# Kernel optimization log

Hardware: AMD Instinct MI355X
Metric: run time of the kernel (lower is better)

## Reference

```python
import jax, jax.numpy as jnp
import numpy as np

H = 128            # hardcoded image side in the torch module
TOL = 1e-3         # forward() default tol
MAX_DEPTH = 8      # init kwarg (reduced from 200 for bounded runtime)
LRELU = 0.1        # LeakyReLU negative slope


def _conv(x, w, b, pad):
    # x: [B,Cin,H,H], w: [Cout,Cin,kh,kw]
    y = jax.lax.conv_general_dilated(
        x, w, (1, 1), [(pad, pad), (pad, pad)],
        dimension_numbers=('NCHW', 'OIHW', 'NCHW'))
    if b is not None:
        y = y + b[None, :, None, None]
    return y


def _leaky(x):
    return jnp.where(x >= 0, x, LRELU * x)


def _build_apply_T(d, A, w1, b1, w2, b2, w3, b3, wK, delta, alpha, lambd, beta):
    B = d.shape[0]
    Kc = wK.shape[0]
    dcol = d.reshape(B, -1).T                      # [m, B]
    # ConvTranspose2d(K->1, k=3, pad=1) with weight := convK.weight is the
    # adjoint of convK: regular conv with spatially flipped, channel-swapped kernel.
    wKt = jnp.transpose(jnp.flip(wK, (2, 3)), (1, 0, 2, 3))  # [1,K,3,3]

    def K_op(xk):                                  # [N,B] -> [K*N,B]
        x4 = xk.T.reshape(B, 1, H, H)
        return _conv(x4, wK, None, 1).reshape(B, -1).T

    def Kt_op(pk):                                 # [K*N,B] -> [N,B]
        p4 = pk.T.reshape(B, Kc, H, H)
        return _conv(p4, wKt, None, 1).reshape(B, -1).T

    def R_op(pk):                                  # learned residual denoiser
        p = pk.T.reshape(B, Kc, H, H)
        p = p + _leaky(_conv(p, w1, b1, 2))
        p = p + _leaky(_conv(p, w2, b2, 2))
        p = p + _leaky(_conv(p, w3, b3, 2))
        return p.reshape(B, -1).T

    def ball_proj(w):                              # eval-mode projection
        de = jnp.exp(delta)                        # (1,) -> broadcasts over batch
        dist = jnp.maximum(jnp.linalg.norm(w - dcol, axis=0), 1e-10)
        dn = jnp.linalg.norm(dcol, axis=0)
        scale = jnp.minimum(jnp.ones_like(dist), de * dn / dist)
        return dcol + scale * (w - dcol)

    a = jnp.clip(alpha, 0.0, 2.0)
    bta = jnp.clip(beta, 0.0, 2.0)
    lam = jnp.clip(lambd, 0.0, 2.0)

    def apply_T(x):                                # x: [B,1,H,H]
        xk = x.reshape(B, -1).T                    # [N,B]
        Kxk = K_op(xk)
        # torch: pk = K(xk); pk += lambd*(nuk1 + alpha*(K(xk)-pk)) with nuk1=0
        # and pk==K(xk), so the update is identity -> pk = Kxk.
        pk = R_op(Kxk)
        Axk = A @ xk                               # [m,B]
        # torch: wk = A@xk; temp = wk + lambd*(nuk2 + alpha*(Axk-wk)) = Axk.
        wk = ball_proj(Axk)
        nuk1p = a * (Kxk - pk)
        nuk2p = a * (Axk - wk)
        # nuk1 = nuk2 = 0, so 2*nuk_plus - nuk = 2*nuk_plus
        rk = Kt_op(2.0 * nuk1p) + A.T @ (2.0 * nuk2p)
        xk_new = jnp.clip(xk - bta * rk, 0.0, 1.0)
        return xk_new.T.reshape(B, 1, H, H)

    return apply_T


def setup_inputs() -> dict:
    key = jax.random.key(0)
    ks = jax.random.split(key, 10)
    B, M, N_side, Kc = 8, 4096, 128, 2
    d = jax.random.normal(ks[0], (B, M), jnp.float32)
    A = jax.random.normal(ks[1], (M, N_side * N_side), jnp.float32) / 128.0
    w1 = jax.random.normal(ks[2], (Kc, Kc, 5, 5), jnp.float32) * 0.05
    w2 = jax.random.normal(ks[3], (Kc, Kc, 5, 5), jnp.float32) * 0.05
    w3 = jax.random.normal(ks[4], (Kc, Kc, 5, 5), jnp.float32) * 0.05
    b1 = jnp.zeros((Kc,), jnp.float32)
    b2 = jnp.zeros((Kc,), jnp.float32)
    b3 = jnp.zeros((Kc,), jnp.float32)
    wK = jax.random.normal(ks[5], (Kc, 1, 3, 3), jnp.float32) * 0.1
    return {
        'd': d, 'A': A,
        'w1': w1, 'b1': b1, 'w2': w2, 'b2': b2, 'w3': w3, 'b3': b3,
        'wK': wK,
        'delta': jnp.full((1,), -5.0, jnp.float32),
        'alpha': jnp.full((1,), 0.1, jnp.float32),
        'lambd': jnp.full((1,), 0.1, jnp.float32),
        'beta': jnp.full((1,), 0.1, jnp.float32),
    }


def reference(d, A, w1, b1, w2, b2, w3, b3, wK, delta, alpha, lambd, beta):
    B = d.shape[0]
    apply_T = _build_apply_T(d, A, w1, b1, w2, b2, w3, b3, wK,
                             delta, alpha, lambd, beta)
    x0 = jnp.zeros((B, 1, H, H), d.dtype)
    xp0 = jnp.full((B, 1, H, H), jnp.inf, d.dtype)

    def cond(state):
        x, xp, k = state
        res = jnp.max(jnp.linalg.norm((x - xp).reshape(B, -1), axis=1))
        return (res > TOL) & (k < MAX_DEPTH)

    def body(state):
        x, xp, k = state
        return (apply_T(x), x, k + 1)

    x_star, _, _ = jax.lax.while_loop(cond, body, (x0, xp0, jnp.int32(0)))
    # final differentiable application T(x*)
    return apply_T(x_star)
```

## Files before the change

kernel.cpp:

```cpp
#include <hip/hip_runtime.h>
#include <math.h>

#define HH 128
#define NPIX 16384
#define BB 8
#define MM 4096
#define NN 16384
#define LRELU_S 0.1f

typedef __attribute__((ext_vector_type(8))) short bf16x8;
typedef __attribute__((ext_vector_type(4))) float f32x4;

__device__ __forceinline__ float leaky_(float v){ return v >= 0.f ? v : LRELU_S*v; }
__device__ __forceinline__ float clamp01(float v){ return fminf(fmaxf(v, 0.f), 1.f); }
__device__ __forceinline__ float clamp02(float v){ return fminf(fmaxf(v, 0.f), 2.f); }
__device__ __forceinline__ unsigned short f2bf(float f){
  unsigned u = __float_as_uint(f);
  u = (u + 0x7FFFu + ((u >> 16) & 1u)) >> 16;
  return (unsigned short)u;
}
__device__ __forceinline__ float bf2f(unsigned short s){
  return __uint_as_float(((unsigned)s) << 16);
}

__global__ __launch_bounds__(256) void k_prep_pack(const float* __restrict__ A_,
                                                   unsigned short* __restrict__ Apk){
  __shared__ unsigned short lb[16][1032];
  int blk = blockIdx.x;
  int mt = blk >> 4, ch = blk & 15;
  int t = threadIdx.x;
  #pragma unroll
  for (int i=0;i<16;++i){
    float4 v = *(const float4*)&A_[(size_t)(mt*16+i)*NN + ch*1024 + t*4];
    unsigned short o[4] = {f2bf(v.x),f2bf(v.y),f2bf(v.z),f2bf(v.w)};
    *(uint2*)&lb[i][t*4] = *(uint2*)o;
  }
  __syncthreads();
  size_t base = ((size_t)mt*2048 + ch*128)*128;
  #pragma unroll
  for (int j=0;j<8;++j){
    int o = j*256 + t;
    int k8l = o >> 4, col = o & 15;
    uint4 v = *(const uint4*)&lb[col][k8l*8];
    *(uint4*)&Apk[base + (size_t)o*8] = v;
  }
}

__global__ __launch_bounds__(256) void k_dn(const float* __restrict__ d, float* __restrict__ dn){
  int b = blockIdx.x, t = threadIdx.x;
  float ss = 0.f;
  for (int m=t; m<MM; m+=256){ float v = d[b*MM + m]; ss += v*v; }
  #pragma unroll
  for (int off=32; off; off>>=1) ss += __shfl_down(ss, off);
  __shared__ float red[4];
  if ((t & 63) == 0) red[t>>6] = ss;
  __syncthreads();
  if (t == 0) dn[b] = sqrtf(red[0]+red[1]+red[2]+red[3]);
}

__global__ __launch_bounds__(256) void k_gemm1p(const unsigned short* __restrict__ Apk,
    const unsigned short* __restrict__ xtt, float* __restrict__ e_part){
  __shared__ float part[4][16][16];
  int blk = blockIdx.x;
  int mt = blk >> 2, ng = blk & 3;
  int t = threadIdx.x, w = t >> 6, lane = t & 63;
  int kg = lane >> 4, col = lane & 15;
  const unsigned short* Ap = Apk + (((size_t)mt*2048 + ng*512 + w*128 + kg)*16 + col)*8;
  const unsigned short* Bp = xtt + ((size_t)(ng*512 + w*128 + kg)*16 + col)*8;
  f32x4 acc = {0.f,0.f,0.f,0.f};
  #pragma unroll 8
  for (int s=0; s<32; ++s){
    bf16x8 a = *(const bf16x8*)(Ap + s*512);
    bf16x8 b = *(const bf16x8*)(Bp + s*512);
    acc = __builtin_amdgcn_mfma_f32_16x16x32_bf16(a, b, acc, 0, 0, 0);
  }
  #pragma unroll
  for (int j=0;j<4;++j) part[w][kg*4+j][col] = acc[j];
  __syncthreads();
  int r = t >> 4, b = t & 15;
  float s = part[0][r][b] + part[1][r][b] + part[2][r][b] + part[3][r][b];
  e_part[((size_t)ng*MM + mt*16 + r)*16 + b] = s;
}

__global__ __launch_bounds__(256) void k_conv_chain(const float* __restrict__ x,
    const float* __restrict__ wK, const float* __restrict__ w1, const float* __restrict__ b1,
    const float* __restrict__ w2, const float* __restrict__ b2,
    const float* __restrict__ w3, const float* __restrict__ b3,
    const float* __restrict__ alpha, float* __restrict__ rk){
  __shared__ float xs[24][128];
  __shared__ float bufA[2][22][128];
  __shared__ float bufB[2][18][128];
  __shared__ float wKs[18], w1s[100], w2s[100], w3s[100], bs[3][2];
  __shared__ float twoa;
  int blk = blockIdx.x;
  int b = blk >> 4, slab = blk & 15, r0 = slab*8;
  int t = threadIdx.x;
  for (int i=t;i<18;i+=256) wKs[i]=wK[i];
  for (int i=t;i<100;i+=256){ w1s[i]=w1[i]; w2s[i]=w2[i]; w3s[i]=w3[i]; }
  if (t<2){ bs[0][t]=b1[t]; bs[1][t]=b2[t]; bs[2][t]=b3[t]; }
  if (t==0) twoa = 2.f*clamp02(alpha[0]);
  for (int idx=t; idx<24*128; idx+=256){
    int i = idx>>7, j = idx&127, ir = r0-8+i;
    xs[i][j] = ((unsigned)ir < 128u) ? x[b*NPIX + ir*HH + j] : 0.f;
  }
  __syncthreads();
  for (int c=0;c<2;++c)
    for (int idx=t; idx<22*128; idx+=256){
      int i = idx>>7, j = idx&127, ir = r0-7+i;
      float s = 0.f;
      if ((unsigned)ir < 128u){
        #pragma unroll
        for (int di=0;di<3;++di)
          #pragma unroll
          for (int dj=0;dj<3;++dj){
            int jj = j+dj-1;
            if ((unsigned)jj < 128u) s += xs[i+di][jj]*wKs[(c*3+di)*3+dj];
          }
      }
      bufA[c][i][j] = s;
    }
  __syncthreads();
  for (int o=0;o<2;++o)
    for (int idx=t; idx<18*128; idx+=256){
      int i = idx>>7, j = idx&127, ir = r0-5+i;
      float v = 0.f;
      if ((unsigned)ir < 128u){
        float s = bs[0][o];
        #pragma unroll
        for (int c=0;c<2;++c)
          #pragma unroll
          for (int di=0;di<5;++di)
            #pragma unroll
            for (int dj=0;dj<5;++dj){
              int jj = j+dj-2;
              if ((unsigned)jj < 128u) s += bufA[c][i+di][jj]*w1s[(o*2+c)*25+di*5+dj];
            }
        v = bufA[o][i+2][j] + leaky_(s);
      }
      bufB[o][i][j] = v;
    }
  __syncthreads();
  for (int o=0;o<2;++o)
    for (int idx=t; idx<14*128; idx+=256){
      int i = idx>>7, j = idx&127, ir = r0-3+i;
      float v = 0.f;
      if ((unsigned)ir < 128u){
        float s = bs[1][o];
        #pragma unroll
        for (int c=0;c<2;++c)
          #pragma unroll
          for (int di=0;di<5;++di)
            #pragma unroll
            for (int dj=0;dj<5;++dj){
              int jj = j+dj-2;
              if ((unsigned)jj < 128u) s += bufB[c][i+di][jj]*w2s[(o*2+c)*25+di*5+dj];
            }
        v = bufB[o][i+2][j] + leaky_(s);
      }
      bufA[o][i][j] = v;
    }
  __syncthreads();
  for (int o=0;o<2;++o)
    for (int idx=t; idx<10*128; idx+=256){
      int i = idx>>7, j = idx&127, ir = r0-1+i;
      float v = 0.f;
      if ((unsigned)ir < 128u){
        float s = bs[2][o];
        #pragma unroll
        for (int c=0;c<2;++c)
          #pragma unroll
          for (int di=0;di<5;++di)
            #pragma unroll
            for (int dj=0;dj<5;++dj){
              int jj = j+dj-2;
              if ((unsigned)jj < 128u) s += bufA[c][i+di][jj]*w3s[(o*2+c)*25+di*5+dj];
            }
        v = bufA[o][i+2][j] + leaky_(s);
      }
      bufB[o][i][j] = v;
    }
  __syncthreads();
  for (int c=0;c<2;++c)
    for (int idx=t; idx<10*128; idx+=256){
      int i = idx>>7, j = idx&127, ir = r0-1+i;
      float v = 0.f;
      if ((unsigned)ir < 128u){
        float kx = 0.f;
        #pragma unroll
        for (int di=0;di<3;++di)
          #pragma unroll
          for (int dj=0;dj<3;++dj){
            int jj = j+dj-1;
            if ((unsigned)jj < 128u) kx += xs[i+6+di][jj]*wKs[(c*3+di)*3+dj];
          }
        v = twoa*(kx - bufB[c][i][j]);
      }
      bufA[c][i][j] = v;
    }
  __syncthreads();
  for (int idx=t; idx<8*128; idx+=256){
    int i = idx>>7, j = idx&127, ir = r0+i;
    float s = 0.f;
    #pragma unroll
    for (int c=0;c<2;++c)
      #pragma unroll
      for (int di=0;di<3;++di)
        #pragma unroll
        for (int dj=0;dj<3;++dj){
          int jj = j+dj-1;
          if ((unsigned)jj < 128u) s += bufA[c][i+di][jj]*wKs[(c*3+(2-di))*3+(2-dj)];
        }
    rk[b*NPIX + ir*HH + j] = s;
  }
}

__global__ __launch_bounds__(256) void k_gemm2a(const unsigned short* __restrict__ Apk,
    const float* __restrict__ e_part, const float* __restrict__ d_,
    float* __restrict__ up, float* __restrict__ d2p){
  __shared__ float zs[8][512];
  __shared__ float red8s[64];
  int blk = blockIdx.x;
  int msp = blk >> 8, nb = blk & 255;
  int m0 = msp*512, mt0 = msp*32, k80 = nb*8;
  int t = threadIdx.x;
  for (int i=t; i<4096; i+=256){
    int ml = i >> 3, b = i & 7;
    int m = m0 + ml;
    float s = e_part[(size_t)(0*MM + m)*16 + b]
            + e_part[(size_t)(1*MM + m)*16 + b]
            + e_part[(size_t)(2*MM + m)*16 + b]
            + e_part[(size_t)(3*MM + m)*16 + b];
    zs[b][ml] = s - d_[b*MM + m];
  }
  __syncthreads();
  if (nb == 0){
    if (t < 64){
      int b = t & 7, g = t >> 3;
      float s = 0.f;
      #pragma unroll
      for (int i=0;i<64;++i){ float v = zs[b][g*64+i]; s += v*v; }
      red8s[g*8 + b] = s;
    }
    __syncthreads();
    if (t < 8){
      float s2 = 0.f;
      #pragma unroll
      for (int g=0;g<8;++g) s2 += red8s[g*8 + t];
      d2p[msp*8 + t] = s2;
    }
  }
  int col = t & 15, ehalf = (t >> 4) & 1, k8l = t >> 5;
  int k8 = k80 + k8l;
  const unsigned short* Ap = Apk + ((((size_t)mt0*2048 + k8)*16 + col)*8 + ehalf*4);
  float acc[8][4];
  #pragma unroll
  for (int b=0;b<8;++b)
    #pragma unroll
    for (int e=0;e<4;++e) acc[b][e] = 0.f;
  for (int mb=0; mb<32; mb+=4){
    uint2 a4[4];
    #pragma unroll
    for (int u=0;u<4;++u)
      a4[u] = *(const uint2*)(Ap + (size_t)(mb+u)*262144);
    #pragma unroll
    for (int u=0;u<4;++u){
      float av[4];
      av[0] = bf2f((unsigned short)(a4[u].x & 0xffff));
      av[1] = bf2f((unsigned short)(a4[u].x >> 16));
      av[2] = bf2f((unsigned short)(a4[u].y & 0xffff));
      av[3] = bf2f((unsigned short)(a4[u].y >> 16));
      int ml = (mb+u)*16 + col;
      #pragma unroll
      for (int b=0;b<8;++b){
        float z = zs[b][ml];
        acc[b][0] += av[0]*z; acc[b][1] += av[1]*z;
        acc[b][2] += av[2]*z; acc[b][3] += av[3]*z;
      }
    }
  }
  #pragma unroll
  for (int mask=1; mask<16; mask<<=1)
    #pragma unroll
    for (int b=0;b<8;++b)
      #pragma unroll
      for (int e=0;e<4;++e) acc[b][e] += __shfl_xor(acc[b][e], mask);
  if (col < 8){
    int b = col;
    float4 v = {acc[b][0], acc[b][1], acc[b][2], acc[b][3]};
    *(float4*)&up[((size_t)msp*8 + b)*NN + k8*8 + ehalf*4] = v;
  }
}

__global__ __launch_bounds__(256) void k_combine3(const float* __restrict__ up,
    const float* __restrict__ rk1, const float* __restrict__ d2p,
    const float* __restrict__ dn, const float* __restrict__ delta,
    const float* __restrict__ alpha, const float* __restrict__ beta,
    float* __restrict__ x, unsigned short* __restrict__ xtt){
  __shared__ float cf_s[8];
  int t = threadIdx.x;
  if (t < 8){
    float s2 = 0.f;
    #pragma unroll
    for (int ms=0; ms<8; ++ms) s2 += d2p[ms*8 + t];
    float dist = fmaxf(sqrtf(s2), 1e-10f);
    float de = expf(delta[0]);
    float a = clamp02(alpha[0]);
    cf_s[t] = 2.f*a*(1.f - fminf(1.f, de*dn[t]/dist));
  }
  __syncthreads();
  float bta = clamp02(beta[0]);
  int o = blockIdx.x*256 + t;
  int b = o >> 14, pix = o & 16383;
  float s = 0.f;
  #pragma unroll
  for (int p=0; p<8; ++p)
    s += up[((size_t)p*8 + b)*NN + pix];
  float tot = rk1[b*NPIX + pix] + cf_s[b]*s;
  float xn = clamp01(x[b*NPIX + pix] - bta*tot);
  x[b*NPIX + pix] = xn;
  xtt[((size_t)(pix>>3)*16 + b)*8 + (pix&7)] = f2bf(xn);
}

extern "C" void kernel_launch(void* const* d_in, const int* in_sizes, int n_in,
                              void* d_out, int out_size, void* d_ws, size_t ws_size,
                              hipStream_t stream) {
  const float* d_d   = (const float*)d_in[0];
  const float* d_A   = (const float*)d_in[1];
  const float* w1    = (const float*)d_in[2];
  const float* b1    = (const float*)d_in[3];
  const float* w2    = (const float*)d_in[4];
  const float* b2    = (const float*)d_in[5];
  const float* w3    = (const float*)d_in[6];
  const float* b3    = (const float*)d_in[7];
  const float* wK    = (const float*)d_in[8];
  const float* delta = (const float*)d_in[9];
  const float* alpha = (const float*)d_in[10];
  const float* beta  = (const float*)d_in[12];

  char* p = (char*)d_ws;
  unsigned short* Apk = (unsigned short*)p; p += (size_t)MM*NN*2;
  unsigned short* xtt = (unsigned short*)p; p += (size_t)2048*16*8*2;
  float* x      = (float*)p; p += (size_t)BB*NPIX*4;
  float* rk1    = (float*)p; p += (size_t)BB*NPIX*4;
  float* e_part = (float*)p; p += (size_t)4*MM*16*4;
  float* up     = (float*)p; p += (size_t)8*8*NN*4;
  float* d2p    = (float*)p; p += (size_t)8*8*4;
  float* dnb    = (float*)p; p += 64;

  k_prep_pack<<<4096, 256, 0, stream>>>(d_A, Apk);
  k_dn<<<BB, 256, 0, stream>>>(d_d, dnb);
  hipMemsetAsync(x, 0, (size_t)BB*NPIX*4, stream);
  hipMemsetAsync(xtt, 0, (size_t)2048*16*8*2, stream);

  for (int it=0; it<9; ++it){
    k_conv_chain<<<128, 256, 0, stream>>>(x, wK, w1, b1, w2, b2, w3, b3, alpha, rk1);
    k_gemm1p<<<1024, 256, 0, stream>>>(Apk, xtt, e_part);
    k_gemm2a<<<2048, 256, 0, stream>>>(Apk, e_part, d_d, up, d2p);
    k_combine3<<<512, 256, 0, stream>>>(up, rk1, d2p, dnb, delta, alpha, beta, x, xtt);
  }

  hipMemcpyAsync(d_out, x, (size_t)BB*NPIX*4, hipMemcpyDeviceToDevice, stream);
}
```

Before: 1.492 ms.

## Merge conv chain with GEMM1 in one launch, store conv buffers as bf16, widen GEMM2 tiles

The denoiser conv chain and the first GEMM now run as one launch, with block ranges split between the two roles, so one launch is removed per iteration and both can run concurrently. The conv chain's shared-memory intermediates are stored as bf16 to shrink LDS use, which allows higher occupancy but lowers precision in the residual chain. GEMM2 now gives each thread 8 output columns instead of 4, which halves the grid and makes the A loads wider, at the cost of more accumulator registers.

```diff
diff --git a/kernel.cpp b/kernel.cpp
--- a/kernel.cpp
+++ b/kernel.cpp
@@ -58,50 +58,56 @@
   if (t == 0) dn[b] = sqrtf(red[0]+red[1]+red[2]+red[3]);
 }
 
-__global__ __launch_bounds__(256) void k_gemm1p(const unsigned short* __restrict__ Apk,
-    const unsigned short* __restrict__ xtt, float* __restrict__ e_part){
-  __shared__ float part[4][16][16];
-  int blk = blockIdx.x;
-  int mt = blk >> 2, ng = blk & 3;
-  int t = threadIdx.x, w = t >> 6, lane = t & 63;
-  int kg = lane >> 4, col = lane & 15;
-  const unsigned short* Ap = Apk + (((size_t)mt*2048 + ng*512 + w*128 + kg)*16 + col)*8;
-  const unsigned short* Bp = xtt + ((size_t)(ng*512 + w*128 + kg)*16 + col)*8;
-  f32x4 acc = {0.f,0.f,0.f,0.f};
-  #pragma unroll 8
-  for (int s=0; s<32; ++s){
-    bf16x8 a = *(const bf16x8*)(Ap + s*512);
-    bf16x8 b = *(const bf16x8*)(Bp + s*512);
-    acc = __builtin_amdgcn_mfma_f32_16x16x32_bf16(a, b, acc, 0, 0, 0);
-  }
-  #pragma unroll
-  for (int j=0;j<4;++j) part[w][kg*4+j][col] = acc[j];
-  __syncthreads();
-  int r = t >> 4, b = t & 15;
-  float s = part[0][r][b] + part[1][r][b] + part[2][r][b] + part[3][r][b];
-  e_part[((size_t)ng*MM + mt*16 + r)*16 + b] = s;
-}
-
-__global__ __launch_bounds__(256) void k_conv_chain(const float* __restrict__ x,
+#define XS(i,j)   xsB[(i)*128+(j)]
+#define BA(c,i,j) bufAB[((c)*22+(i))*128+(j)]
+#define BBD(c,i,j) bufBB[((c)*18+(i))*128+(j)]
+
+__global__ __launch_bounds__(256) void k_g1c(const unsigned short* __restrict__ Apk,
+    const unsigned short* __restrict__ xtt, const float* __restrict__ x,
     const float* __restrict__ wK, const float* __restrict__ w1, const float* __restrict__ b1,
     const float* __restrict__ w2, const float* __restrict__ b2,
     const float* __restrict__ w3, const float* __restrict__ b3,
-    const float* __restrict__ alpha, float* __restrict__ rk){
-  __shared__ float xs[24][128];
-  __shared__ float bufA[2][22][128];
-  __shared__ float bufB[2][18][128];
-  __shared__ float wKs[18], w1s[100], w2s[100], w3s[100], bs[3][2];
-  __shared__ float twoa;
-  int blk = blockIdx.x;
-  int b = blk >> 4, slab = blk & 15, r0 = slab*8;
-  int t = threadIdx.x;
+    const float* __restrict__ alpha,
+    float* __restrict__ e_part, float* __restrict__ rk1){
+  __shared__ float smem[6656];
+  __shared__ float wKs[18], w1s[100], w2s[100], w3s[100], bs[6];
+  int blk = blockIdx.x, t = threadIdx.x;
+
+  if (blk < 1024){
+    float* part = smem;
+    int mt = blk >> 2, ng = blk & 3;
+    int w = t >> 6, lane = t & 63;
+    int kg = lane >> 4, col = lane & 15;
+    const unsigned short* Ap = Apk + (((size_t)mt*2048 + ng*512 + w*128 + kg)*16 + col)*8;
+    const unsigned short* Bp = xtt + ((size_t)(ng*512 + w*128 + kg)*16 + col)*8;
+    f32x4 acc = {0.f,0.f,0.f,0.f};
+    #pragma unroll 8
+    for (int s=0; s<32; ++s){
+      bf16x8 a = *(const bf16x8*)(Ap + s*512);
+      bf16x8 b = *(const bf16x8*)(Bp + s*512);
+      acc = __builtin_amdgcn_mfma_f32_16x16x32_bf16(a, b, acc, 0, 0, 0);
+    }
+    #pragma unroll
+    for (int j=0;j<4;++j) part[w*256 + (kg*4+j)*16 + col] = acc[j];
+    __syncthreads();
+    int r = t >> 4, b = t & 15;
+    float s = part[r*16+b] + part[256+r*16+b] + part[512+r*16+b] + part[768+r*16+b];
+    e_part[((size_t)ng*MM + mt*16 + r)*16 + b] = s;
+    return;
+  }
+
+  unsigned short* xsB   = (unsigned short*)&smem[0];
+  unsigned short* bufAB = (unsigned short*)&smem[1536];
+  unsigned short* bufBB = (unsigned short*)&smem[4352];
+  int cb = blk - 1024;
+  int b = cb >> 4, slab = cb & 15, r0 = slab*8;
+  float twoa = 2.f*clamp02(alpha[0]);
   for (int i=t;i<18;i+=256) wKs[i]=wK[i];
   for (int i=t;i<100;i+=256){ w1s[i]=w1[i]; w2s[i]=w2[i]; w3s[i]=w3[i]; }
-  if (t<2){ bs[0][t]=b1[t]; bs[1][t]=b2[t]; bs[2][t]=b3[t]; }
-  if (t==0) twoa = 2.f*clamp02(alpha[0]);
+  if (t<2){ bs[t]=b1[t]; bs[2+t]=b2[t]; bs[4+t]=b3[t]; }
   for (int idx=t; idx<24*128; idx+=256){
     int i = idx>>7, j = idx&127, ir = r0-8+i;
-    xs[i][j] = ((unsigned)ir < 128u) ? x[b*NPIX + ir*HH + j] : 0.f;
+    XS(i,j) = f2bf(((unsigned)ir < 128u) ? x[b*NPIX + ir*HH + j] : 0.f);
   }
   __syncthreads();
   for (int c=0;c<2;++c)
@@ -114,10 +120,10 @@
           #pragma unroll
           for (int dj=0;dj<3;++dj){
             int jj = j+dj-1;
-            if ((unsigned)jj < 128u) s += xs[i+di][jj]*wKs[(c*3+di)*3+dj];
+            if ((unsigned)jj < 128u) s += bf2f(XS(i+di,jj))*wKs[(c*3+di)*3+dj];
           }
       }
-      bufA[c][i][j] = s;
+      BA(c,i,j) = f2bf(s);
     }
   __syncthreads();
   for (int o=0;o<2;++o)
@@ -125,7 +131,7 @@
       int i = idx>>7, j = idx&127, ir = r0-5+i;
       float v = 0.f;
       if ((unsigned)ir < 128u){
-        float s = bs[0][o];
+        float s = bs[o];
         #pragma unroll
         for (int c=0;c<2;++c)
           #pragma unroll
@@ -133,11 +139,11 @@
             #pragma unroll
             for (int dj=0;dj<5;++dj){
               int jj = j+dj-2;
-              if ((unsigned)jj < 128u) s += bufA[c][i+di][jj]*w1s[(o*2+c)*25+di*5+dj];
+              if ((unsigned)jj < 128u) s += bf2f(BA(c,i+di,jj))*w1s[(o*2+c)*25+di*5+dj];
             }
-        v = bufA[o][i+2][j] + leaky_(s);
-      }
-      bufB[o][i][j] = v;
+        v = bf2f(BA(o,i+2,j)) + leaky_(s);
+      }
+      BBD(o,i,j) = f2bf(v);
     }
   __syncthreads();
   for (int o=0;o<2;++o)
@@ -145,7 +151,7 @@
       int i = idx>>7, j = idx&127, ir = r0-3+i;
       float v = 0.f;
       if ((unsigned)ir < 128u){
-        float s = bs[1][o];
+        float s = bs[2+o];
         #pragma unroll
         for (int c=0;c<2;++c)
           #pragma unroll
@@ -153,11 +159,11 @@
             #pragma unroll
             for (int dj=0;dj<5;++dj){
               int jj = j+dj-2;
-              if ((unsigned)jj < 128u) s += bufB[c][i+di][jj]*w2s[(o*2+c)*25+di*5+dj];
+              if ((unsigned)jj < 128u) s += bf2f(BBD(c,i+di,jj))*w2s[(o*2+c)*25+di*5+dj];
             }
-        v = bufB[o][i+2][j] + leaky_(s);
-      }
-      bufA[o][i][j] = v;
+        v = bf2f(BBD(o,i+2,j)) + leaky_(s);
+      }
+      BA(o,i,j) = f2bf(v);
     }
   __syncthreads();
   for (int o=0;o<2;++o)
@@ -165,7 +171,7 @@
       int i = idx>>7, j = idx&127, ir = r0-1+i;
       float v = 0.f;
       if ((unsigned)ir < 128u){
-        float s = bs[2][o];
+        float s = bs[4+o];
         #pragma unroll
         for (int c=0;c<2;++c)
           #pragma unroll
@@ -173,11 +179,11 @@
             #pragma unroll
             for (int dj=0;dj<5;++dj){
               int jj = j+dj-2;
-              if ((unsigned)jj < 128u) s += bufA[c][i+di][jj]*w3s[(o*2+c)*25+di*5+dj];
+              if ((unsigned)jj < 128u) s += bf2f(BA(c,i+di,jj))*w3s[(o*2+c)*25+di*5+dj];
             }
-        v = bufA[o][i+2][j] + leaky_(s);
-      }
-      bufB[o][i][j] = v;
+        v = bf2f(BA(o,i+2,j)) + leaky_(s);
+      }
+      BBD(o,i,j) = f2bf(v);
     }
   __syncthreads();
   for (int c=0;c<2;++c)
@@ -191,11 +197,11 @@
           #pragma unroll
           for (int dj=0;dj<3;++dj){
             int jj = j+dj-1;
-            if ((unsigned)jj < 128u) kx += xs[i+6+di][jj]*wKs[(c*3+di)*3+dj];
+            if ((unsigned)jj < 128u) kx += bf2f(XS(i+6+di,jj))*wKs[(c*3+di)*3+dj];
           }
-        v = twoa*(kx - bufB[c][i][j]);
-      }
-      bufA[c][i][j] = v;
+        v = twoa*(kx - bf2f(BBD(c,i,j)));
+      }
+      BA(c,i,j) = f2bf(v);
     }
   __syncthreads();
   for (int idx=t; idx<8*128; idx+=256){
@@ -208,20 +214,20 @@
         #pragma unroll
         for (int dj=0;dj<3;++dj){
           int jj = j+dj-1;
-          if ((unsigned)jj < 128u) s += bufA[c][i+di][jj]*wKs[(c*3+(2-di))*3+(2-dj)];
+          if ((unsigned)jj < 128u) s += bf2f(BA(c,i+di,jj))*wKs[(c*3+(2-di))*3+(2-dj)];
         }
-    rk[b*NPIX + ir*HH + j] = s;
-  }
-}
-
-__global__ __launch_bounds__(256) void k_gemm2a(const unsigned short* __restrict__ Apk,
+    rk1[b*NPIX + ir*HH + j] = s;
+  }
+}
+
+__global__ __launch_bounds__(256) void k_gemm2b(const unsigned short* __restrict__ Apk,
     const float* __restrict__ e_part, const float* __restrict__ d_,
     float* __restrict__ up, float* __restrict__ d2p){
   __shared__ float zs[8][512];
   __shared__ float red8s[64];
   int blk = blockIdx.x;
-  int msp = blk >> 8, nb = blk & 255;
-  int m0 = msp*512, mt0 = msp*32, k80 = nb*8;
+  int msp = blk >> 7, nb = blk & 127;
+  int m0 = msp*512, mt0 = msp*32, k80 = nb*16;
   int t = threadIdx.x;
   for (int i=t; i<4096; i+=256){
     int ml = i >> 3, b = i & 7;
@@ -249,32 +255,32 @@
       d2p[msp*8 + t] = s2;
     }
   }
-  int col = t & 15, ehalf = (t >> 4) & 1, k8l = t >> 5;
+  int col = t & 15, k8l = t >> 4;
   int k8 = k80 + k8l;
-  const unsigned short* Ap = Apk + ((((size_t)mt0*2048 + k8)*16 + col)*8 + ehalf*4);
-  float acc[8][4];
+  const unsigned short* Ap = Apk + (((size_t)mt0*2048 + k8)*16 + col)*8;
+  float acc[8][8];
   #pragma unroll
   for (int b=0;b<8;++b)
     #pragma unroll
-    for (int e=0;e<4;++e) acc[b][e] = 0.f;
+    for (int e=0;e<8;++e) acc[b][e] = 0.f;
   for (int mb=0; mb<32; mb+=4){
-    uint2 a4[4];
+    uint4 a4[4];
     #pragma unroll
     for (int u=0;u<4;++u)
-      a4[u] = *(const uint2*)(Ap + (size_t)(mb+u)*262144);
+      a4[u] = *(const uint4*)(Ap + (size_t)(mb+u)*262144);
     #pragma unroll
     for (int u=0;u<4;++u){
-      float av[4];
-      av[0] = bf2f((unsigned short)(a4[u].x & 0xffff));
-      av[1] = bf2f((unsigned short)(a4[u].x >> 16));
-      av[2] = bf2f((unsigned short)(a4[u].y & 0xffff));
-      av[3] = bf2f((unsigned short)(a4[u].y >> 16));
+      float av[8];
+      av[0]=bf2f((unsigned short)(a4[u].x & 0xffff)); av[1]=bf2f((unsigned short)(a4[u].x >> 16));
+      av[2]=bf2f((unsigned short)(a4[u].y & 0xffff)); av[3]=bf2f((unsigned short)(a4[u].y >> 16));
+      av[4]=bf2f((unsigned short)(a4[u].z & 0xffff)); av[5]=bf2f((unsigned short)(a4[u].z >> 16));
+      av[6]=bf2f((unsigned short)(a4[u].w & 0xffff)); av[7]=bf2f((unsigned short)(a4[u].w >> 16));
       int ml = (mb+u)*16 + col;
       #pragma unroll
       for (int b=0;b<8;++b){
         float z = zs[b][ml];
-        acc[b][0] += av[0]*z; acc[b][1] += av[1]*z;
-        acc[b][2] += av[2]*z; acc[b][3] += av[3]*z;
+        #pragma unroll
+        for (int e=0;e<8;++e) acc[b][e] += av[e]*z;
       }
     }
   }
@@ -283,11 +289,14 @@
     #pragma unroll
     for (int b=0;b<8;++b)
       #pragma unroll
-      for (int e=0;e<4;++e) acc[b][e] += __shfl_xor(acc[b][e], mask);
+      for (int e=0;e<8;++e) acc[b][e] += __shfl_xor(acc[b][e], mask);
   if (col < 8){
     int b = col;
-    float4 v = {acc[b][0], acc[b][1], acc[b][2], acc[b][3]};
-    *(float4*)&up[((size_t)msp*8 + b)*NN + k8*8 + ehalf*4] = v;
+    float4 v0 = {acc[b][0], acc[b][1], acc[b][2], acc[b][3]};
+    float4 v1 = {acc[b][4], acc[b][5], acc[b][6], acc[b][7]};
+    float* dst = &up[((size_t)msp*8 + b)*NN + k8*8];
+    *(float4*)dst = v0;
+    *(float4*)(dst+4) = v1;
   }
 }
 
@@ -353,9 +362,9 @@
   hipMemsetAsync(xtt, 0, (size_t)2048*16*8*2, stream);
 
   for (int it=0; it<9; ++it){
-    k_conv_chain<<<128, 256, 0, stream>>>(x, wK, w1, b1, w2, b2, w3, b3, alpha, rk1);
-    k_gemm1p<<<1024, 256, 0, stream>>>(Apk, xtt, e_part);
-    k_gemm2a<<<2048, 256, 0, stream>>>(Apk, e_part, d_d, up, d2p);
+    k_g1c<<<1152, 256, 0, stream>>>(Apk, xtt, x, wK, w1, b1, w2, b2, w3, b3,
+                                    alpha, e_part, rk1);
+    k_gemm2b<<<1024, 256, 0, stream>>>(Apk, e_part, d_d, up, d2p);
     k_combine3<<<512, 256, 0, stream>>>(up, rk1, d2p, dnb, delta, alpha, beta, x, xtt);
   }
 
```

Result: slower. 1.680 ms (+12.6%).
